# Performance work log

Hardware: AMD Instinct MI355X
Metric: run time of the kernel (lower is better)

The kernel has to match this reference:

```python
import jax, jax.numpy as jnp
import numpy as np

TAU_MEM = 20.0          # tau for both ExpLeak (syn) and LIF (mem)
SPIKE_THRESHOLD = 1.0
WIDTH_GRAD = 0.5        # surrogate gradient width (unused in fwd)
SCALE_GRAD = 1.0


def setup_inputs() -> dict:
    key = jax.random.key(0)
    k1, k2 = jax.random.split(key)
    x = jax.random.normal(k1, (32, 2048, 512, 1), dtype=jnp.float32)
    weight = jax.random.uniform(k2, (1, 1), dtype=jnp.float32)  # Linear(1,1,bias=False) weight (set to scalar `weight` in torch)
    return {"x": x, "weight": weight}


def reference(x, weight):
    # x: (B, T, N, 1); weight: (1, 1)
    alpha = jnp.exp(jnp.asarray(-1.0 / TAU_MEM, dtype=x.dtype))
    i_in = x * weight[0, 0]                      # Linear(1,1,no bias)
    i_in = jnp.moveaxis(i_in, 1, 0)              # (T, B, N, 1) for scan over time

    def step(carry, i_t):
        v_syn, v_mem = carry
        # ExpLeak, norm_input=False: v_syn = alpha*v_syn + input
        v_syn = alpha * v_syn + i_t
        # LIF, norm_input=False: decay then integrate synaptic current
        v_mem = alpha * v_mem + v_syn
        # SingleSpike: at most one spike per step
        spk = (v_mem >= SPIKE_THRESHOLD).astype(v_mem.dtype)
        # MembraneSubtract reset
        v_mem = v_mem - SPIKE_THRESHOLD * spk
        return (v_syn, v_mem), spk

    zeros = jnp.zeros_like(i_in[0])
    _, spikes = jax.lax.scan(step, (zeros, zeros), i_in)
    return jnp.moveaxis(spikes, 0, 1)            # (B, T, N, 1)
```

## Files before the change

### kernel.cpp

```cpp
#include <hip/hip_runtime.h>
#include <math.h>


constexpr int B_ = 32;
constexpr int T_ = 2048;
constexpr int N_ = 512;
constexpr int TILE = 64;
constexpr int NTILE = T_ / TILE;
constexpr int NCHUNK = 64;
constexpr int NPROD = 4;
constexpr int RPP = TILE / NPROD;

__global__ __launch_bounds__(320, 1)
void exodus_pc_kernel(const float* __restrict__ x,
                      const float* __restrict__ wptr,
                      float* __restrict__ out) {
    __shared__ float XBUF[2][TILE][NCHUNK];
    __shared__ float SBUF[2][TILE][NCHUNK];

    const int blk  = blockIdx.x;
    const int b    = blk >> 3;
    const int n0   = (blk & 7) * NCHUNK;
    const int wave = threadIdx.x >> 6;
    const int lane = threadIdx.x & 63;

    const size_t base = (size_t)b * T_ * N_ + (size_t)n0 + lane;
    const float* __restrict__ xp = x + base;
    float* __restrict__ op = out + base;

    if (wave != 0) {
        const int p  = wave - 1;
        const int j0 = p * RPP;

        {
            const float* __restrict__ g = xp + (size_t)j0 * N_;
            float r[RPP];
#pragma unroll
            for (int i = 0; i < RPP; ++i) r[i] = g[(size_t)i * N_];
#pragma unroll
            for (int i = 0; i < RPP; ++i) XBUF[0][j0 + i][lane] = r[i];
        }
        __syncthreads();

        for (int t = 0; t <= NTILE; ++t) {
            if (t + 1 < NTILE) {
                const float* __restrict__ g =
                    xp + ((size_t)(t + 1) * TILE + j0) * N_;
                const int bb = (t + 1) & 1;
                float r[RPP];
#pragma unroll
                for (int i = 0; i < RPP; ++i) r[i] = g[(size_t)i * N_];
#pragma unroll
                for (int i = 0; i < RPP; ++i) XBUF[bb][j0 + i][lane] = r[i];
            }
            if (t >= 1) {
                float* __restrict__ o =
                    op + ((size_t)(t - 1) * TILE + j0) * N_;
                const int bb = (t - 1) & 1;
                float s[RPP];
#pragma unroll
                for (int i = 0; i < RPP; ++i) s[i] = SBUF[bb][j0 + i][lane];
#pragma unroll
                for (int i = 0; i < RPP; ++i) o[(size_t)i * N_] = s[i];
            }
            __syncthreads();
        }
    } else {
        const float w = wptr[0];
        const float alpha = (float)exp((double)(-1.0f / 20.0f));
        float vsyn = 0.0f, vmem = 0.0f;

        __syncthreads();

        for (int t = 0; t <= NTILE; ++t) {
            if (t < NTILE) {
                const int bb = t & 1;
                float xv[TILE];
#pragma unroll
                for (int j = 0; j < TILE; ++j)
                    xv[j] = XBUF[bb][j][lane];
#pragma unroll
                for (int j = 0; j < TILE; ++j) {
                    const float i_t = __fmul_rn(xv[j], w);
                    vsyn = __fadd_rn(__fmul_rn(alpha, vsyn), i_t);
                    const float va = __fadd_rn(__fmul_rn(alpha, vmem), vsyn);
                    const bool fire = (va >= 1.0f);
                    SBUF[bb][j][lane] = fire ? 1.0f : 0.0f;
                    vmem = fire ? __fsub_rn(va, 1.0f) : va;
                }
            }
            __syncthreads();
        }
    }
}

extern "C" void kernel_launch(void* const* d_in, const int* in_sizes, int n_in,
                              void* d_out, int out_size, void* d_ws, size_t ws_size,
                              hipStream_t stream) {
    const float* x = (const float*)d_in[0];
    const float* w = (const float*)d_in[1];
    float* out = (float*)d_out;

    dim3 grid(256);
    dim3 block(320);
    hipLaunchKernelGGL(exodus_pc_kernel, grid, block, 0, stream, x, w, out);
}
```

Baseline: 237.8 us.

## Replace producer-consumer LDS pipeline with single-wave register double buffering

Drops the four producer waves and the shared-memory staging buffers. Each block is now a single 64-lane wave that double-buffers 32-step input tiles in registers and writes spikes straight to global memory with nontemporal stores. This removes LDS traffic and block-wide barriers on the serial scan path. In exchange each wave has less memory parallelism in flight and uses more registers, and the grid still only has 256 single-wave blocks to hide global memory latency.

```diff
diff --git a/kernel.cpp b/kernel.cpp
--- a/kernel.cpp
+++ b/kernel.cpp
@@ -5,91 +5,68 @@
 constexpr int B_ = 32;
 constexpr int T_ = 2048;
 constexpr int N_ = 512;
-constexpr int TILE = 64;
-constexpr int NTILE = T_ / TILE;
-constexpr int NCHUNK = 64;
-constexpr int NPROD = 4;
-constexpr int RPP = TILE / NPROD;
+constexpr int TILE = 32;
+constexpr int NT = T_ / TILE;
 
-__global__ __launch_bounds__(320, 1)
-void exodus_pc_kernel(const float* __restrict__ x,
-                      const float* __restrict__ wptr,
-                      float* __restrict__ out) {
-    __shared__ float XBUF[2][TILE][NCHUNK];
-    __shared__ float SBUF[2][TILE][NCHUNK];
-
+__global__ __launch_bounds__(64, 1)
+void exodus_direct_kernel(const float* __restrict__ x,
+                          const float* __restrict__ wptr,
+                          float* __restrict__ out) {
     const int blk  = blockIdx.x;
     const int b    = blk >> 3;
-    const int n0   = (blk & 7) * NCHUNK;
-    const int wave = threadIdx.x >> 6;
-    const int lane = threadIdx.x & 63;
+    const int n0   = (blk & 7) * 64;
+    const int lane = threadIdx.x;
 
     const size_t base = (size_t)b * T_ * N_ + (size_t)n0 + lane;
     const float* __restrict__ xp = x + base;
     float* __restrict__ op = out + base;
 
-    if (wave != 0) {
-        const int p  = wave - 1;
-        const int j0 = p * RPP;
+    const float w = wptr[0];
+    const float alpha = (float)exp((double)(-1.0f / 20.0f));
 
+    float bufA[TILE], bufB[TILE];
+
+#pragma unroll
+    for (int i = 0; i < TILE; ++i) bufA[i] = xp[(size_t)i * N_];
+
+    float vsyn = 0.0f, vmem = 0.0f;
+
+    for (int t = 0; t < NT; t += 2) {
         {
-            const float* __restrict__ g = xp + (size_t)j0 * N_;
-            float r[RPP];
+            const float* __restrict__ g = xp + (size_t)(t + 1) * TILE * N_;
 #pragma unroll
-            for (int i = 0; i < RPP; ++i) r[i] = g[(size_t)i * N_];
+            for (int i = 0; i < TILE; ++i) bufB[i] = g[(size_t)i * N_];
+        }
+        {
+            float* __restrict__ o = op + (size_t)t * TILE * N_;
 #pragma unroll
-            for (int i = 0; i < RPP; ++i) XBUF[0][j0 + i][lane] = r[i];
+            for (int j = 0; j < TILE; ++j) {
+                const float i_t = __fmul_rn(bufA[j], w);
+                vsyn = __fadd_rn(__fmul_rn(alpha, vsyn), i_t);
+                const float va = __fadd_rn(__fmul_rn(alpha, vmem), vsyn);
+                const bool fire = (va >= 1.0f);
+                __builtin_nontemporal_store(fire ? 1.0f : 0.0f,
+                                            o + (size_t)j * N_);
+                vmem = fire ? __fsub_rn(va, 1.0f) : va;
+            }
         }
-        __syncthreads();
-
-        for (int t = 0; t <= NTILE; ++t) {
-            if (t + 1 < NTILE) {
-                const float* __restrict__ g =
-                    xp + ((size_t)(t + 1) * TILE + j0) * N_;
-                const int bb = (t + 1) & 1;
-                float r[RPP];
+        if (t + 2 < NT) {
+            const float* __restrict__ g = xp + (size_t)(t + 2) * TILE * N_;
 #pragma unroll
-                for (int i = 0; i < RPP; ++i) r[i] = g[(size_t)i * N_];
+            for (int i = 0; i < TILE; ++i) bufA[i] = g[(size_t)i * N_];
+        }
+        {
+            float* __restrict__ o = op + (size_t)(t + 1) * TILE * N_;
 #pragma unroll
-                for (int i = 0; i < RPP; ++i) XBUF[bb][j0 + i][lane] = r[i];
+            for (int j = 0; j < TILE; ++j) {
+                const float i_t = __fmul_rn(bufB[j], w);
+                vsyn = __fadd_rn(__fmul_rn(alpha, vsyn), i_t);
+                const float va = __fadd_rn(__fmul_rn(alpha, vmem), vsyn);
+                const bool fire = (va >= 1.0f);
+                __builtin_nontemporal_store(fire ? 1.0f : 0.0f,
+                                            o + (size_t)j * N_);
+                vmem = fire ? __fsub_rn(va, 1.0f) : va;
             }
-            if (t >= 1) {
-                float* __restrict__ o =
-                    op + ((size_t)(t - 1) * TILE + j0) * N_;
-                const int bb = (t - 1) & 1;
-                float s[RPP];
-#pragma unroll
-                for (int i = 0; i < RPP; ++i) s[i] = SBUF[bb][j0 + i][lane];
-#pragma unroll
-                for (int i = 0; i < RPP; ++i) o[(size_t)i * N_] = s[i];
-            }
-            __syncthreads();
-        }
-    } else {
-        const float w = wptr[0];
-        const float alpha = (float)exp((double)(-1.0f / 20.0f));
-        float vsyn = 0.0f, vmem = 0.0f;
-
-        __syncthreads();
-
-        for (int t = 0; t <= NTILE; ++t) {
-            if (t < NTILE) {
-                const int bb = t & 1;
-                float xv[TILE];
-#pragma unroll
-                for (int j = 0; j < TILE; ++j)
-                    xv[j] = XBUF[bb][j][lane];
-#pragma unroll
-                for (int j = 0; j < TILE; ++j) {
-                    const float i_t = __fmul_rn(xv[j], w);
-                    vsyn = __fadd_rn(__fmul_rn(alpha, vsyn), i_t);
-                    const float va = __fadd_rn(__fmul_rn(alpha, vmem), vsyn);
-                    const bool fire = (va >= 1.0f);
-                    SBUF[bb][j][lane] = fire ? 1.0f : 0.0f;
-                    vmem = fire ? __fsub_rn(va, 1.0f) : va;
-                }
-            }
-            __syncthreads();
         }
     }
 }
@@ -102,6 +79,6 @@
     float* out = (float*)d_out;
 
     dim3 grid(256);
-    dim3 block(320);
-    hipLaunchKernelGGL(exodus_pc_kernel, grid, block, 0, stream, x, w, out);
+    dim3 block(64);
+    hipLaunchKernelGGL(exodus_direct_kernel, grid, block, 0, stream, x, w, out);
 }
```

After: 258.6 us. +8.7%, slower.
